# Performance work log

Hardware: AMD Instinct MI355X
Metric: run time of the kernel (lower is better)

Reference implementation:

```python
import jax, jax.numpy as jnp
import numpy as np

B, T, D, H, WIN, G = 2, 2048, 768, 12, 16, 32
HD = D // H            # 64
K = 2 * WIN + 1        # local kernel size = 33


def setup_inputs() -> dict:
    key = jax.random.key(0)
    ks = jax.random.split(key, 5)
    s = 1.0 / np.sqrt(D).astype(np.float32)
    x = jax.random.normal(ks[0], (B, T, D), jnp.float32)
    # first G tokens of every batch are global (matches original's nonzero(global_mask[b]))
    global_mask = jnp.zeros((B, T), jnp.int32).at[:, :G].set(1)
    Wq = jax.random.normal(ks[1], (D, D), jnp.float32) * s
    Wk = jax.random.normal(ks[2], (D, D), jnp.float32) * s
    Wv = jax.random.normal(ks[3], (D, D), jnp.float32) * s
    Wo = jax.random.normal(ks[4], (D, D), jnp.float32) * s
    bq = jnp.zeros((D,), jnp.float32)
    bk = jnp.zeros((D,), jnp.float32)
    bv = jnp.zeros((D,), jnp.float32)
    bo = jnp.zeros((D,), jnp.float32)
    return {"x": x, "global_mask": global_mask, "Wq": Wq, "bq": bq,
            "Wk": Wk, "bk": bk, "Wv": Wv, "bv": bv, "Wo": Wo, "bo": bo}


def reference(x, global_mask, Wq, bq, Wk, bk, Wv, bv, Wo, bo):
    def split_heads(y):
        return y.reshape(B, T, H, HD).transpose(0, 2, 1, 3)  # [B,H,T,HD]

    q = split_heads(x @ Wq + bq)
    k = split_heads(x @ Wk + bk)
    v = split_heads(x @ Wv + bv)

    scale = 1.0 / np.sqrt(HD).astype(np.float32)

    offs = jnp.arange(-WIN, WIN + 1)
    idx = jnp.arange(T)[:, None] + offs[None, :]          # [T,K]
    valid = (idx >= 0) & (idx < T)                        # [T,K]
    idxc = jnp.clip(idx, 0, T - 1)

    k_loc = k[:, :, idxc]                                 # [B,H,T,K,HD]
    s_loc = jnp.einsum('bhtd,bhtkd->bhtk', q, k_loc) * scale
    s_loc = jnp.where(valid, s_loc, -jnp.inf)             # out-of-range excluded from softmax

    # global tokens (same positions for every batch by construction)
    g_idx = jnp.nonzero(global_mask[0], size=G)[0]        # [G]
    k_g = k[:, :, g_idx]                                  # [B,H,G,HD]
    v_g = v[:, :, g_idx]
    s_g = jnp.einsum('bhtd,bhgd->bhtg', q, k_g) * scale   # [B,H,T,G]

    # joint softmax over [local window, global tokens] (globals in window are double-counted,
    # exactly as in the original torch.cat([local_s, g_score]))
    attn = jax.nn.softmax(jnp.concatenate([s_loc, s_g], axis=-1), axis=-1)
    a_loc = jnp.where(valid, attn[..., :K], 0.0)          # [B,H,T,K]
    a_g = attn[..., K:]                                   # [B,H,T,G]

    v_loc = v[:, :, idxc]                                 # [B,H,T,K,HD]
    ctx = (jnp.einsum('bhtk,bhtkd->bhtd', a_loc, v_loc)
           + jnp.einsum('bhtg,bhgd->bhtd', a_g, v_g))     # [B,H,T,HD]

    out = ctx.transpose(0, 2, 1, 3).reshape(B, T, D) @ Wo + bo

    # dense attention map: scatter local band (add; invalid entries are 0),
    # then overwrite global columns (matches original write order)
    rows = jnp.arange(T)[:, None]                         # [T,1]
    full_attn = jnp.zeros((B, H, T, T), jnp.float32)
    full_attn = full_attn.at[:, :, rows, idxc].add(a_loc)
    full_attn = full_attn.at[:, :, :, g_idx].set(a_g)
    return out, full_attn
```

## Files before the change

### kernel.cpp

```cpp
#include <hip/hip_runtime.h>

typedef unsigned short u16;
typedef __attribute__((ext_vector_type(4))) u16 u16x4;
typedef __attribute__((ext_vector_type(8))) u16 u16x8;
typedef __attribute__((ext_vector_type(8))) short bf16x8;
typedef __attribute__((ext_vector_type(4))) float f32x4;

#define BB 2
#define TT 2048
#define DD 768
#define NH 12
#define HDIM 64
#define NQKV 2304
#define MM 4096

__device__ __forceinline__ u16 f2bf(float f) {
  unsigned u = __float_as_uint(f);
  u += 0x7fffu + ((u >> 16) & 1u);
  return (u16)(u >> 16);
}
__device__ __forceinline__ float bf2f(u16 s) {
  return __uint_as_float(((unsigned)s) << 16);
}
__device__ __forceinline__ void async_load16(const void* g, void* l) {
  __builtin_amdgcn_global_load_lds((const __attribute__((address_space(1))) void*)g,
                                   (__attribute__((address_space(3))) void*)l, 16, 0, 0);
}

__global__ __launch_bounds__(256) void castx(const float* __restrict__ x, u16* __restrict__ xb) {
  int i = blockIdx.x * 256 + threadIdx.x;
  float4 v = ((const float4*)x)[i];
  u16x4 o = { f2bf(v.x), f2bf(v.y), f2bf(v.z), f2bf(v.w) };
  ((u16x4*)xb)[i] = o;
}

__global__ __launch_bounds__(256) void wprep(const float* __restrict__ Wq, const float* __restrict__ Wk,
                                             const float* __restrict__ Wv, const float* __restrict__ Wo,
                                             u16* __restrict__ wqkvT, u16* __restrict__ woT) {
  __shared__ float tile[32][33];
  int z = blockIdx.z;
  const float* W = (z == 0) ? Wq : (z == 1) ? Wk : (z == 2) ? Wv : Wo;
  u16* dst = (z < 3) ? (wqkvT + (size_t)z * DD * DD) : woT;
  int k0 = blockIdx.x * 32, n0 = blockIdx.y * 32;
  int tx = threadIdx.x, ty = threadIdx.y;
#pragma unroll
  for (int j = 0; j < 4; ++j)
    tile[ty + j * 8][tx] = W[(size_t)(k0 + ty + j * 8) * DD + n0 + tx];
  __syncthreads();
#pragma unroll
  for (int j = 0; j < 4; ++j)
    dst[(size_t)(n0 + ty + j * 8) * DD + k0 + tx] = f2bf(tile[tx][ty + j * 8]);
}

__global__ __launch_bounds__(256) void prep_misc(const int* __restrict__ gm,
                                                 const float* __restrict__ bq, const float* __restrict__ bk,
                                                 const float* __restrict__ bv,
                                                 int* __restrict__ gidx, int* __restrict__ gpos,
                                                 float* __restrict__ biasqkv) {
  int tid = threadIdx.x;
  if (tid < 32) gidx[tid] = 0;
  for (int c = tid; c < TT; c += 256) gpos[c] = -1;
  for (int n = tid; n < NQKV; n += 256)
    biasqkv[n] = (n < 768) ? bq[n] : (n < 1536) ? bk[n - 768] : bv[n - 1536];
  __syncthreads();
  if (tid < 64) {
    int lane = tid;
    int base = 0;
    for (int c0 = 0; c0 < TT; c0 += 64) {
      int mval = gm[c0 + lane];
      unsigned long long bal = __ballot(mval != 0);
      int pre = __popcll(bal & ((1ull << lane) - 1ull));
      if (mval && (base + pre) < 32) { gidx[base + pre] = c0 + lane; gpos[c0 + lane] = base + pre; }
      base += __popcll(bal);
      if (base >= 32) break;
    }
  }
}

template <int BM, bool OUTBF>
__global__ __launch_bounds__(256) void gemm_bt(const u16* __restrict__ A, const u16* __restrict__ BT,
                                               const float* __restrict__ bias, void* __restrict__ Cv,
                                               int Ndim, int Kd) {
  constexpr int NJ = (BM == 128) ? 4 : 2;
  constexpr int ACH = BM / 32;
  __shared__ __attribute__((aligned(16))) u16 As[BM * 64];
  __shared__ __attribute__((aligned(16))) u16 Bs[128 * 64];
  const int tid = threadIdx.x;
  const int wave = tid >> 6, lane = tid & 63;
  const int m0 = blockIdx.x * BM, n0 = blockIdx.y * 128;
  const int wm = (BM == 128) ? ((wave & 1) << 6) : 0;
  const int wn = (BM == 128) ? ((wave >> 1) << 6) : (wave << 5);
  const int lr = lane & 15, lk = lane >> 4;
  const int srow_b = lane >> 3;
  const int scol = (lane & 7) * 8;

  f32x4 acc[4][NJ] = {};

  const int kIters = Kd >> 6;
  for (int kt = 0; kt < kIters; ++kt) {
#pragma unroll
    for (int cc = 0; cc < ACH; ++cc) {
      int c = wave * ACH + cc;
      int srow = c * 8 + srow_b;
      async_load16(A + (size_t)(m0 + srow) * Kd + (kt << 6) + scol, (void*)(As + c * 512));
    }
#pragma unroll
    for (int cc = 0; cc < 4; ++cc) {
      int c = wave * 4 + cc;
      int srow = c * 8 + srow_b;
      async_load16(BT + (size_t)(n0 + srow) * Kd + (kt << 6) + scol, (void*)(Bs + c * 512));
    }
    __syncthreads();
#pragma unroll
    for (int kc = 0; kc < 2; ++kc) {
      bf16x8 af[4], bfr[NJ];
#pragma unroll
      for (int i = 0; i < 4; ++i)
        af[i] = *(const bf16x8*)(As + (wm + i * 16 + lr) * 64 + kc * 32 + lk * 8);
#pragma unroll
      for (int j = 0; j < NJ; ++j)
        bfr[j] = *(const bf16x8*)(Bs + (wn + j * 16 + lr) * 64 + kc * 32 + lk * 8);
#pragma unroll
      for (int i = 0; i < 4; ++i)
#pragma unroll
        for (int j = 0; j < NJ; ++j)
          acc[i][j] = __builtin_amdgcn_mfma_f32_16x16x32_bf16(af[i], bfr[j], acc[i][j], 0, 0, 0);
    }
    __syncthreads();
  }

#pragma unroll
  for (int i = 0; i < 4; ++i) {
    const int row = m0 + wm + i * 16 + lk * 4;
#pragma unroll
    for (int j = 0; j < NJ; ++j) {
      const int col = n0 + wn + j * 16 + lr;
      const float bs = bias[col];
#pragma unroll
      for (int r = 0; r < 4; ++r) {
        const float val = acc[i][j][r] + bs;
        if (OUTBF) ((u16*)Cv)[(size_t)(row + r) * Ndim + col] = f2bf(val);
        else       ((float*)Cv)[(size_t)(row + r) * Ndim + col] = val;
      }
    }
  }
}

__global__ __launch_bounds__(256) void attn_kernel(const u16* __restrict__ qb,
                                                   const int* __restrict__ gidx,
                                                   const int* __restrict__ gpos,
                                                   u16* __restrict__ ctxb,
                                                   float* __restrict__ fattn) {
  __shared__ __attribute__((aligned(16))) u16 Kl[96 * 72];
  __shared__ __attribute__((aligned(16))) u16 Kg[32 * 72];
  __shared__ __attribute__((aligned(16))) u16 Vl[96 * 72];
  __shared__ __attribute__((aligned(16))) u16 Vg[32 * 72];
  __shared__ __attribute__((aligned(16))) float probs[64 * 68];
  __shared__ int wgpos[96];
  __shared__ int gidxs[32];

  const int tid = threadIdx.x;
  const int blk = blockIdx.x;
  const int chunk = blk & 31;
  const int h = (blk >> 5) % NH;
  const int b = blk / 384;
  const int t0 = chunk << 6;

  {
    const int r = tid >> 3;
    const int c8 = (tid & 7) << 3;
#pragma unroll
    for (int it = 0; it < 3; ++it) {
      int rr = it * 32 + r;
      int t = t0 - 16 + rr;
      t = t < 0 ? 0 : (t > TT - 1 ? TT - 1 : t);
      const u16* src = qb + (size_t)(b * TT + t) * NQKV + h * HDIM + c8;
      *(u16x8*)(Kl + rr * 72 + c8) = *(const u16x8*)(src + 768);
      *(u16x8*)(Vl + rr * 72 + c8) = *(const u16x8*)(src + 1536);
    }
    {
      int t = gidx[r];
      const u16* src = qb + (size_t)(b * TT + t) * NQKV + h * HDIM + c8;
      *(u16x8*)(Kg + r * 72 + c8) = *(const u16x8*)(src + 768);
      *(u16x8*)(Vg + r * 72 + c8) = *(const u16x8*)(src + 1536);
    }
    if (tid < 32) gidxs[tid] = gidx[tid];
    if (tid < 96) {
      int t = t0 - 16 + tid;
      wgpos[tid] = ((unsigned)t < TT) ? gpos[t] : -1;
    }
  }
  __syncthreads();

  const int tl = tid >> 2, sub = tid & 3;
  const int t = t0 + tl;
  const u16* qp = qb + (size_t)(b * TT + t) * NQKV + h * HDIM;
  float qv[64];
#pragma unroll
  for (int i = 0; i < 8; ++i) {
    u16x8 qq = *(const u16x8*)(qp + i * 8);
#pragma unroll
    for (int e = 0; e < 8; ++e) qv[i * 8 + e] = bf2f(qq[e]);
  }

  float sc[17];
  float mmax = -__builtin_inff();
#pragma unroll
  for (int i = 0; i < 17; ++i) {
    const int s = sub + (i << 2);
    const u16* kp;
    bool valid;
    if (s < 33) { kp = Kl + (tl + s) * 72; int j = t - 16 + s; valid = (j >= 0) && (j < TT); }
    else if (s < 65) { kp = Kg + (s - 33) * 72; valid = true; }
    else { kp = Kg; valid = false; }
    float d = 0.f;
#pragma unroll
    for (int i2 = 0; i2 < 8; ++i2) {
      u16x8 kv = *(const u16x8*)(kp + i2 * 8);
#pragma unroll
      for (int e = 0; e < 8; ++e) d += qv[i2 * 8 + e] * bf2f(kv[e]);
    }
    sc[i] = valid ? d * 0.125f : -__builtin_inff();
    mmax = fmaxf(mmax, sc[i]);
  }
  mmax = fmaxf(mmax, __shfl_xor(mmax, 1));
  mmax = fmaxf(mmax, __shfl_xor(mmax, 2));
  float sum = 0.f;
#pragma unroll
  for (int i = 0; i < 17; ++i) { sc[i] = __expf(sc[i] - mmax); sum += sc[i]; }
  sum += __shfl_xor(sum, 1);
  sum += __shfl_xor(sum, 2);
  const float inv = 1.0f / sum;
#pragma unroll
  for (int i = 0; i < 17; ++i) {
    const int s = sub + (i << 2);
    sc[i] *= inv;
    if (s < 65) probs[tl * 68 + s] = sc[i];
  }
  __syncthreads();

  float cacc[16];
#pragma unroll
  for (int i = 0; i < 16; ++i) cacc[i] = 0.f;
#pragma unroll 1
  for (int k = 0; k < 65; ++k) {
    const float pv = probs[tl * 68 + k];
    const u16* vp = (k < 33) ? (Vl + (tl + k) * 72) : (Vg + (k - 33) * 72);
    const u16* vq = vp + (sub << 4);
    u16x8 v0 = *(const u16x8*)(vq);
    u16x8 v1 = *(const u16x8*)(vq + 8);
#pragma unroll
    for (int e = 0; e < 8; ++e) { cacc[e] += pv * bf2f(v0[e]); cacc[8 + e] += pv * bf2f(v1[e]); }
  }
  {
    u16x8 cb0, cb1;
#pragma unroll
    for (int e = 0; e < 8; ++e) { cb0[e] = f2bf(cacc[e]); cb1[e] = f2bf(cacc[8 + e]); }
    u16* dst = ctxb + (size_t)(b * TT + t) * DD + h * HDIM + (sub << 4);
    *(u16x8*)dst = cb0;
    *(u16x8*)(dst + 8) = cb1;
  }

  float* fbase = fattn + ((size_t)(b * NH + h) * TT + t0) * TT;
#pragma unroll 1
  for (int it = 0; it < 128; ++it) {
    int f = it * 256 + tid;
    int rl = f >> 9;
    int c4 = (f & 511) << 2;
    int trow = t0 + rl;
    float4 v = make_float4(0.f, 0.f, 0.f, 0.f);
    int kk = c4 - trow + 16;
    if (kk >= -3 && kk < 33) {
      const float* pr = probs + rl * 68;
      float* vp = &v.x;
#pragma unroll
      for (int e = 0; e < 4; ++e) {
        int k2 = kk + e;
        if ((unsigned)k2 < 33u) vp[e] = pr[k2];
      }
    }
    *(float4*)(fbase + (size_t)rl * TT + c4) = v;
  }
  __syncthreads();

  {
    int rl = tid >> 2, g0 = (tid & 3) << 3;
    const float* pr = probs + rl * 68 + 33;
    float* frow = fbase + (size_t)rl * TT;
#pragma unroll
    for (int e = 0; e < 8; ++e) frow[gidxs[g0 + e]] = pr[g0 + e];
  }
}

extern "C" void kernel_launch(void* const* d_in, const int* in_sizes, int n_in,
                              void* d_out, int out_size, void* d_ws, size_t ws_size,
                              hipStream_t stream) {
  const float* x  = (const float*)d_in[0];
  const int* gm   = (const int*)d_in[1];
  const float* Wq = (const float*)d_in[2];
  const float* bq = (const float*)d_in[3];
  const float* Wk = (const float*)d_in[4];
  const float* bk = (const float*)d_in[5];
  const float* Wv = (const float*)d_in[6];
  const float* bv = (const float*)d_in[7];
  const float* Wo = (const float*)d_in[8];
  const float* bo = (const float*)d_in[9];

  float* out = (float*)d_out;
  float* fattn = out + (size_t)BB * TT * DD;

  char* p = (char*)d_ws;
  u16* xb      = (u16*)p;  p += (size_t)MM * DD * 2;
  u16* wqkvT   = (u16*)p;  p += (size_t)NQKV * DD * 2;
  u16* woT     = (u16*)p;  p += (size_t)DD * DD * 2;
  float* biasq = (float*)p; p += (size_t)NQKV * 4;
  int* gidx    = (int*)p;  p += 128;
  int* gpos    = (int*)p;  p += (size_t)TT * 4;
  u16* qkvb    = (u16*)p;  p += (size_t)MM * NQKV * 2;
  u16* ctxb    = (u16*)p;  p += (size_t)MM * DD * 2;

  castx<<<MM * DD / 4 / 256, 256, 0, stream>>>(x, xb);
  wprep<<<dim3(24, 24, 4), dim3(32, 8), 0, stream>>>(Wq, Wk, Wv, Wo, wqkvT, woT);
  prep_misc<<<1, 256, 0, stream>>>(gm, bq, bk, bv, gidx, gpos, biasq);
  gemm_bt<128, true><<<dim3(MM / 128, NQKV / 128), 256, 0, stream>>>(xb, wqkvT, biasq, qkvb, NQKV, DD);
  attn_kernel<<<BB * NH * (TT / 64), 256, 0, stream>>>(qkvb, gidx, gpos, ctxb, fattn);
  gemm_bt<64, false><<<dim3(MM / 64, DD / 128), 256, 0, stream>>>(ctxb, woT, bo, out, DD, DD);
}
```

Baseline: 547.9 us.

## Merge prep kernels, store probs as bf16, use nontemporal stores for attention map

Folds the three preprocessing launches (x cast, weight transpose, bias/global index setup) into one kernel and drops the unused gpos array. In the attention kernel, probabilities are kept in shared memory as bf16 instead of fp32, which shrinks LDS use so that three blocks per CU can be requested via launch bounds. The large dense attention-map writes become nontemporal stores to avoid polluting cache. Storing probabilities as bf16 lowers the precision of both the context and the written attention map.

```diff
diff --git a/kernel.cpp b/kernel.cpp
--- a/kernel.cpp
+++ b/kernel.cpp
@@ -27,52 +27,53 @@
                                    (__attribute__((address_space(3))) void*)l, 16, 0, 0);
 }
 
-__global__ __launch_bounds__(256) void castx(const float* __restrict__ x, u16* __restrict__ xb) {
-  int i = blockIdx.x * 256 + threadIdx.x;
-  float4 v = ((const float4*)x)[i];
-  u16x4 o = { f2bf(v.x), f2bf(v.y), f2bf(v.z), f2bf(v.w) };
-  ((u16x4*)xb)[i] = o;
-}
-
-__global__ __launch_bounds__(256) void wprep(const float* __restrict__ Wq, const float* __restrict__ Wk,
-                                             const float* __restrict__ Wv, const float* __restrict__ Wo,
-                                             u16* __restrict__ wqkvT, u16* __restrict__ woT) {
+__global__ __launch_bounds__(256) void prep_all(const float* __restrict__ x,
+                                                const float* __restrict__ Wq, const float* __restrict__ Wk,
+                                                const float* __restrict__ Wv, const float* __restrict__ Wo,
+                                                const int* __restrict__ gm,
+                                                const float* __restrict__ bq, const float* __restrict__ bk,
+                                                const float* __restrict__ bv,
+                                                u16* __restrict__ xb, u16* __restrict__ wqkvT,
+                                                u16* __restrict__ woT,
+                                                int* __restrict__ gidx, float* __restrict__ biasqkv) {
   __shared__ float tile[32][33];
-  int z = blockIdx.z;
-  const float* W = (z == 0) ? Wq : (z == 1) ? Wk : (z == 2) ? Wv : Wo;
-  u16* dst = (z < 3) ? (wqkvT + (size_t)z * DD * DD) : woT;
-  int k0 = blockIdx.x * 32, n0 = blockIdx.y * 32;
-  int tx = threadIdx.x, ty = threadIdx.y;
-#pragma unroll
-  for (int j = 0; j < 4; ++j)
-    tile[ty + j * 8][tx] = W[(size_t)(k0 + ty + j * 8) * DD + n0 + tx];
-  __syncthreads();
-#pragma unroll
-  for (int j = 0; j < 4; ++j)
-    dst[(size_t)(n0 + ty + j * 8) * DD + k0 + tx] = f2bf(tile[tx][ty + j * 8]);
-}
-
-__global__ __launch_bounds__(256) void prep_misc(const int* __restrict__ gm,
-                                                 const float* __restrict__ bq, const float* __restrict__ bk,
-                                                 const float* __restrict__ bv,
-                                                 int* __restrict__ gidx, int* __restrict__ gpos,
-                                                 float* __restrict__ biasqkv) {
-  int tid = threadIdx.x;
-  if (tid < 32) gidx[tid] = 0;
-  for (int c = tid; c < TT; c += 256) gpos[c] = -1;
-  for (int n = tid; n < NQKV; n += 256)
-    biasqkv[n] = (n < 768) ? bq[n] : (n < 1536) ? bk[n - 768] : bv[n - 1536];
-  __syncthreads();
-  if (tid < 64) {
-    int lane = tid;
-    int base = 0;
-    for (int c0 = 0; c0 < TT; c0 += 64) {
-      int mval = gm[c0 + lane];
-      unsigned long long bal = __ballot(mval != 0);
-      int pre = __popcll(bal & ((1ull << lane) - 1ull));
-      if (mval && (base + pre) < 32) { gidx[base + pre] = c0 + lane; gpos[c0 + lane] = base + pre; }
-      base += __popcll(bal);
-      if (base >= 32) break;
+  const int bid = blockIdx.x;
+  const int tid = threadIdx.x;
+  if (bid < 3072) {
+    int i = bid * 256 + tid;
+    float4 v = ((const float4*)x)[i];
+    u16x4 o = { f2bf(v.x), f2bf(v.y), f2bf(v.z), f2bf(v.w) };
+    ((u16x4*)xb)[i] = o;
+  } else if (bid < 5376) {
+    int r = bid - 3072;
+    int z = r / 576; r %= 576;
+    int kx = r % 24, ny = r / 24;
+    const float* W = (z == 0) ? Wq : (z == 1) ? Wk : (z == 2) ? Wv : Wo;
+    u16* dst = (z < 3) ? (wqkvT + (size_t)z * DD * DD) : woT;
+    int k0 = kx * 32, n0 = ny * 32;
+    int tx = tid & 31, ty = tid >> 5;
+#pragma unroll
+    for (int j = 0; j < 4; ++j)
+      tile[ty + j * 8][tx] = W[(size_t)(k0 + ty + j * 8) * DD + n0 + tx];
+    __syncthreads();
+#pragma unroll
+    for (int j = 0; j < 4; ++j)
+      dst[(size_t)(n0 + ty + j * 8) * DD + k0 + tx] = f2bf(tile[tx][ty + j * 8]);
+  } else {
+    for (int n = tid; n < NQKV; n += 256)
+      biasqkv[n] = (n < 768) ? bq[n] : (n < 1536) ? bk[n - 768] : bv[n - 1536];
+    if (tid < 64) {
+      int lane = tid;
+      if (lane < 32) gidx[lane] = 0;
+      int base = 0;
+      for (int c0 = 0; c0 < TT; c0 += 64) {
+        int mval = gm[c0 + lane];
+        unsigned long long bal = __ballot(mval != 0);
+        int pre = __popcll(bal & ((1ull << lane) - 1ull));
+        if (mval && (base + pre) < 32) gidx[base + pre] = c0 + lane;
+        base += __popcll(bal);
+        if (base >= 32) break;
+      }
     }
   }
 }
@@ -146,17 +147,15 @@
   }
 }
 
-__global__ __launch_bounds__(256) void attn_kernel(const u16* __restrict__ qb,
-                                                   const int* __restrict__ gidx,
-                                                   const int* __restrict__ gpos,
-                                                   u16* __restrict__ ctxb,
-                                                   float* __restrict__ fattn) {
+__global__ __launch_bounds__(256, 3) void attn_kernel(const u16* __restrict__ qb,
+                                                      const int* __restrict__ gidx,
+                                                      u16* __restrict__ ctxb,
+                                                      float* __restrict__ fattn) {
   __shared__ __attribute__((aligned(16))) u16 Kl[96 * 72];
   __shared__ __attribute__((aligned(16))) u16 Kg[32 * 72];
   __shared__ __attribute__((aligned(16))) u16 Vl[96 * 72];
   __shared__ __attribute__((aligned(16))) u16 Vg[32 * 72];
-  __shared__ __attribute__((aligned(16))) float probs[64 * 68];
-  __shared__ int wgpos[96];
+  __shared__ __attribute__((aligned(16))) u16 probsB[64 * 68];
   __shared__ int gidxs[32];
 
   const int tid = threadIdx.x;
@@ -185,10 +184,6 @@
       *(u16x8*)(Vg + r * 72 + c8) = *(const u16x8*)(src + 1536);
     }
     if (tid < 32) gidxs[tid] = gidx[tid];
-    if (tid < 96) {
-      int t = t0 - 16 + tid;
-      wgpos[tid] = ((unsigned)t < TT) ? gpos[t] : -1;
-    }
   }
   __syncthreads();
 
@@ -234,8 +229,7 @@
 #pragma unroll
   for (int i = 0; i < 17; ++i) {
     const int s = sub + (i << 2);
-    sc[i] *= inv;
-    if (s < 65) probs[tl * 68 + s] = sc[i];
+    if (s < 65) probsB[tl * 68 + s] = f2bf(sc[i] * inv);
   }
   __syncthreads();
 
@@ -244,7 +238,7 @@
   for (int i = 0; i < 16; ++i) cacc[i] = 0.f;
 #pragma unroll 1
   for (int k = 0; k < 65; ++k) {
-    const float pv = probs[tl * 68 + k];
+    const float pv = bf2f(probsB[tl * 68 + k]);
     const u16* vp = (k < 33) ? (Vl + (tl + k) * 72) : (Vg + (k - 33) * 72);
     const u16* vq = vp + (sub << 4);
     u16x8 v0 = *(const u16x8*)(vq);
@@ -268,27 +262,25 @@
     int rl = f >> 9;
     int c4 = (f & 511) << 2;
     int trow = t0 + rl;
-    float4 v = make_float4(0.f, 0.f, 0.f, 0.f);
+    f32x4 v = {0.f, 0.f, 0.f, 0.f};
     int kk = c4 - trow + 16;
     if (kk >= -3 && kk < 33) {
-      const float* pr = probs + rl * 68;
-      float* vp = &v.x;
 #pragma unroll
       for (int e = 0; e < 4; ++e) {
         int k2 = kk + e;
-        if ((unsigned)k2 < 33u) vp[e] = pr[k2];
+        if ((unsigned)k2 < 33u) v[e] = bf2f(probsB[rl * 68 + k2]);
       }
     }
-    *(float4*)(fbase + (size_t)rl * TT + c4) = v;
+    __builtin_nontemporal_store(v, (f32x4*)(fbase + (size_t)rl * TT + c4));
   }
   __syncthreads();
 
   {
     int rl = tid >> 2, g0 = (tid & 3) << 3;
-    const float* pr = probs + rl * 68 + 33;
     float* frow = fbase + (size_t)rl * TT;
 #pragma unroll
-    for (int e = 0; e < 8; ++e) frow[gidxs[g0 + e]] = pr[g0 + e];
+    for (int e = 0; e < 8; ++e)
+      __builtin_nontemporal_store(bf2f(probsB[rl * 68 + 33 + g0 + e]), frow + gidxs[g0 + e]);
   }
 }
 
@@ -315,14 +307,12 @@
   u16* woT     = (u16*)p;  p += (size_t)DD * DD * 2;
   float* biasq = (float*)p; p += (size_t)NQKV * 4;
   int* gidx    = (int*)p;  p += 128;
-  int* gpos    = (int*)p;  p += (size_t)TT * 4;
   u16* qkvb    = (u16*)p;  p += (size_t)MM * NQKV * 2;
   u16* ctxb    = (u16*)p;  p += (size_t)MM * DD * 2;
 
-  castx<<<MM * DD / 4 / 256, 256, 0, stream>>>(x, xb);
-  wprep<<<dim3(24, 24, 4), dim3(32, 8), 0, stream>>>(Wq, Wk, Wv, Wo, wqkvT, woT);
-  prep_misc<<<1, 256, 0, stream>>>(gm, bq, bk, bv, gidx, gpos, biasq);
+  prep_all<<<5377, 256, 0, stream>>>(x, Wq, Wk, Wv, Wo, gm, bq, bk, bv,
+                                     xb, wqkvT, woT, gidx, biasq);
   gemm_bt<128, true><<<dim3(MM / 128, NQKV / 128), 256, 0, stream>>>(xb, wqkvT, biasq, qkvb, NQKV, DD);
-  attn_kernel<<<BB * NH * (TT / 64), 256, 0, stream>>>(qkvb, gidx, gpos, ctxb, fattn);
+  attn_kernel<<<BB * NH * (TT / 64), 256, 0, stream>>>(qkvb, gidx, ctxb, fattn);
   gemm_bt<64, false><<<dim3(MM / 64, DD / 128), 256, 0, stream>>>(ctxb, woT, bo, out, DD, DD);
 }
```

Result: slower. 584.6 us (+6.7%).
